# Performance work log

Measured on AMD Instinct MI355X. Metric: run time of the kernel, lower is better.

## Reference

```python
import jax, jax.numpy as jnp
import numpy as np

B, S, D = 16, 2048, 128

def setup_inputs() -> dict:
    key = jax.random.key(0)
    kq, kk, kv = jax.random.split(key, 3)
    return {
        "query": jax.random.normal(kq, (B, S, D), dtype=jnp.float32),
        "key": jax.random.normal(kk, (B, S, D), dtype=jnp.float32),
        "value": jax.random.normal(kv, (B, S, D), dtype=jnp.float32),
    }

def reference(query, key, value):
    # query: (B, S2, d), key: (B, S1, d), value: (B, S1, d)
    d_k = query.shape[-1]
    scale = 1.0 / jnp.sqrt(jnp.asarray(d_k, dtype=query.dtype))
    # (B, S2, S1) attention scores
    att = jnp.einsum('bqd,bkd->bqk', query, key) * scale
    att = jax.nn.softmax(att, axis=-1)
    # (B, S2, d_v)
    return jnp.einsum('bqk,bkd->bqd', att, value)
```

## Files before the change

kernel.cpp:

```cpp
#include <hip/hip_runtime.h>

#define B_N 16
#define S_LEN 2048
#define D_DIM 128
#define TK 32
#define NTH 32
#define PSTR 40

typedef __attribute__((ext_vector_type(16))) float f32x16;
typedef __attribute__((ext_vector_type(8)))  short short8;
typedef const __attribute__((address_space(1))) void* gp1;
typedef __attribute__((address_space(3))) void* sp3;
#define GLL(g, l) __builtin_amdgcn_global_load_lds((gp1)(const void*)(g), (sp3)(void*)(l), 16, 0, 0)

static __device__ __forceinline__ unsigned short f2bf(float f) {
  unsigned u = __builtin_bit_cast(unsigned, f);
  return (unsigned short)((u + 0x7fffu + ((u >> 16) & 1u)) >> 16);
}

__global__ __launch_bounds__(256)
void prep_kernel(const float* __restrict__ K, const float* __restrict__ V,
                 unsigned short* __restrict__ Kb, unsigned short* __restrict__ VT) {
  __shared__ unsigned short lds[64 * 66];
  int bx = blockIdx.x;
  int t  = threadIdx.x;
  if (bx < 4096) {
    size_t i = ((size_t)bx * 256 + t) * 4;
    float4 v = *(const float4*)(K + i);
    unsigned lo = (unsigned)f2bf(v.x) | ((unsigned)f2bf(v.y) << 16);
    unsigned hi = (unsigned)f2bf(v.z) | ((unsigned)f2bf(v.w) << 16);
    *(uint2*)(Kb + i) = make_uint2(lo, hi);
  } else {
    int bi = bx - 4096;
    int b  = bi & 15;
    int st = (bi >> 4) & 31;
    int dt = bi >> 9;
    const float* Vb = V + ((size_t)b * S_LEN + st * 64) * D_DIM + dt * 64;
    unsigned short* VTb = VT + ((size_t)b * D_DIM + dt * 64) * S_LEN + st * 64;
#pragma unroll
    for (int rep = 0; rep < 4; ++rep) {
      int idx = rep * 256 + t;
      int i  = idx >> 4;
      int j4 = (idx & 15) * 4;
      float4 v = *(const float4*)(Vb + (size_t)i * D_DIM + j4);
      unsigned lo = (unsigned)f2bf(v.x) | ((unsigned)f2bf(v.y) << 16);
      unsigned hi = (unsigned)f2bf(v.z) | ((unsigned)f2bf(v.w) << 16);
      *(uint2*)&lds[i * 66 + j4] = make_uint2(lo, hi);
    }
    __syncthreads();
#pragma unroll
    for (int rep = 0; rep < 4; ++rep) {
      int idx = rep * 256 + t;
      int dd = idx >> 4;
      int s4 = (idx & 15) * 4;
      unsigned short e0 = lds[(s4 + 0) * 66 + dd];
      unsigned short e1 = lds[(s4 + 1) * 66 + dd];
      unsigned short e2 = lds[(s4 + 2) * 66 + dd];
      unsigned short e3 = lds[(s4 + 3) * 66 + dd];
      *(uint2*)(VTb + (size_t)dd * S_LEN + s4) =
          make_uint2((unsigned)e0 | ((unsigned)e1 << 16),
                     (unsigned)e2 | ((unsigned)e3 << 16));
    }
  }
}

__global__ __launch_bounds__(512, 2)
void attn_kernel(const float* __restrict__ Q, const unsigned short* __restrict__ Kb,
                 const unsigned short* __restrict__ VT, float* __restrict__ O) {
  __shared__ __align__(16) char smem[86016];

  const int tid  = threadIdx.x;
  const int wave = tid >> 6;
  const int g    = wave >> 2;
  const int w4   = wave & 3;
  const int lane = tid & 63;
  const int l32  = lane & 31;
  const int half = lane >> 5;

  const int i     = blockIdx.x;
  const int b     = (i & 7) * 2 + ((i >> 3) & 1);
  const int qtile = i >> 4;
  const int qbase = qtile * 128 + w4 * 32;

  const float* Qb = Q + (size_t)b * S_LEN * D_DIM;
  const unsigned short* Kbb = Kb + (size_t)b * S_LEN * D_DIM;
  const unsigned short* VTb = VT + (size_t)b * D_DIM * S_LEN;

  unsigned short* kb0 = (unsigned short*)smem + (size_t)g * 2 * 4096;
  unsigned short* vb0 = (unsigned short*)(smem + 32768) + (size_t)g * 2 * 4096;
  unsigned short* pw  = (unsigned short*)(smem + 65536) + wave * 32 * PSTR;

  {
    const int T0 = g * NTH;
#pragma unroll
    for (int cc = 0; cc < 2; ++cc) {
      int c = w4 * 2 + cc;
      int rl = 4 * c + (lane >> 4);
      int lbk = (lane & 15) ^ (rl & 15);
      GLL(Kbb + (size_t)(T0 * TK + rl) * D_DIM + lbk * 8, kb0 + c * 512);
      int dv = 16 * c + (lane >> 2);
      int lbv = (lane & 3) ^ ((dv >> 1) & 3);
      GLL(VTb + (size_t)dv * S_LEN + T0 * TK + lbv * 8, vb0 + c * 512);
    }
  }

  short8 qa[8];
  {
    const float* qp = Qb + (size_t)(qbase + l32) * D_DIM + half * 8;
#pragma unroll
    for (int ks = 0; ks < 8; ++ks) {
      float4 a0 = *(const float4*)(qp + ks * 16);
      float4 a1 = *(const float4*)(qp + ks * 16 + 4);
      short8 f;
      f[0] = (short)f2bf(a0.x); f[1] = (short)f2bf(a0.y);
      f[2] = (short)f2bf(a0.z); f[3] = (short)f2bf(a0.w);
      f[4] = (short)f2bf(a1.x); f[5] = (short)f2bf(a1.y);
      f[6] = (short)f2bf(a1.z); f[7] = (short)f2bf(a1.w);
      qa[ks] = f;
    }
  }

  const f32x16 zf16 = {0.f,0.f,0.f,0.f,0.f,0.f,0.f,0.f,0.f,0.f,0.f,0.f,0.f,0.f,0.f,0.f};
  f32x16 oacc[4];
  float lsum[16];
#pragma unroll
  for (int dt = 0; dt < 4; ++dt) oacc[dt] = zf16;
#pragma unroll
  for (int r = 0; r < 16; ++r) lsum[r] = 0.f;

  const float SC = 0.08838834764831845f * 1.4426950408889634f;

  for (int t = 0; t < NTH; ++t) {
    __syncthreads();
    const int cb = t & 1;
    const unsigned short* kbc = kb0 + cb * 4096;
    const unsigned short* vbc = vb0 + cb * 4096;

    if (t + 1 < NTH) {
      const int nb = cb ^ 1;
      const int T = g * NTH + t + 1;
#pragma unroll
      for (int cc = 0; cc < 2; ++cc) {
        int c = w4 * 2 + cc;
        int rl = 4 * c + (lane >> 4);
        int lbk = (lane & 15) ^ (rl & 15);
        GLL(Kbb + (size_t)(T * TK + rl) * D_DIM + lbk * 8, kb0 + nb * 4096 + c * 512);
        int dv = 16 * c + (lane >> 2);
        int lbv = (lane & 3) ^ ((dv >> 1) & 3);
        GLL(VTb + (size_t)dv * S_LEN + T * TK + lbv * 8, vb0 + nb * 4096 + c * 512);
      }
    }

    f32x16 sacc = zf16;
#pragma unroll
    for (int ks = 0; ks < 8; ++ks) {
      int pk = (ks * 2 + half) ^ (l32 & 15);
      short8 kf = *(const short8*)&kbc[l32 * D_DIM + pk * 8];
      sacc = __builtin_amdgcn_mfma_f32_32x32x16_bf16(qa[ks], kf, sacc, 0, 0, 0);
    }

#pragma unroll
    for (int reg = 0; reg < 16; ++reg) {
      float p = exp2f(sacc[reg] * SC);
      lsum[reg] += p;
      int row = (reg & 3) + 8 * (reg >> 2) + 4 * half;
      pw[row * PSTR + l32] = f2bf(p);
    }

    short8 pf[2];
#pragma unroll
    for (int ks2 = 0; ks2 < 2; ++ks2)
      pf[ks2] = *(const short8*)&pw[l32 * PSTR + ks2 * 16 + half * 8];

#pragma unroll
    for (int ks2 = 0; ks2 < 2; ++ks2) {
#pragma unroll
      for (int dt = 0; dt < 4; ++dt) {
        int dv = dt * 32 + l32;
        int pv = (ks2 * 2 + half) ^ ((dv >> 1) & 3);
        short8 vf = *(const short8*)&vbc[dv * TK + pv * 8];
        oacc[dt] = __builtin_amdgcn_mfma_f32_32x32x16_bf16(pf[ks2], vf, oacc[dt], 0, 0, 0);
      }
    }
  }

#pragma unroll
  for (int reg = 0; reg < 16; ++reg) {
    float s = lsum[reg];
    s += __shfl_xor(s, 1);
    s += __shfl_xor(s, 2);
    s += __shfl_xor(s, 4);
    s += __shfl_xor(s, 8);
    s += __shfl_xor(s, 16);
    lsum[reg] = s;
  }

  __syncthreads();
  float* mo = (float*)(smem + w4 * 16512);
  float* ml = (float*)(smem + w4 * 16512 + 16384);
  if (g == 1) {
#pragma unroll
    for (int reg = 0; reg < 16; ++reg) {
      int row = (reg & 3) + 8 * (reg >> 2) + 4 * half;
#pragma unroll
      for (int dt = 0; dt < 4; ++dt)
        mo[row * 128 + dt * 32 + l32] = oacc[dt][reg];
      if (l32 == 0) ml[row] = lsum[reg];
    }
  }
  __syncthreads();
  if (g == 0) {
    float* Ob = O + (size_t)b * S_LEN * D_DIM;
#pragma unroll
    for (int reg = 0; reg < 16; ++reg) {
      int row = (reg & 3) + 8 * (reg >> 2) + 4 * half;
      float linv = 1.f / (lsum[reg] + ml[row]);
#pragma unroll
      for (int dt = 0; dt < 4; ++dt)
        Ob[(size_t)(qbase + row) * D_DIM + dt * 32 + l32] =
            (oacc[dt][reg] + mo[row * 128 + dt * 32 + l32]) * linv;
    }
  }
}

extern "C" void kernel_launch(void* const* d_in, const int* in_sizes, int n_in,
                              void* d_out, int out_size, void* d_ws, size_t ws_size,
                              hipStream_t stream) {
  const float* Q = (const float*)d_in[0];
  const float* K = (const float*)d_in[1];
  const float* V = (const float*)d_in[2];
  float* O = (float*)d_out;
  unsigned short* Kb = (unsigned short*)d_ws;
  unsigned short* VT = Kb + (size_t)B_N * S_LEN * D_DIM;
  prep_kernel<<<dim3(4096 + 1024), dim3(256), 0, stream>>>(K, V, Kb, VT);
  attn_kernel<<<dim3(256), dim3(512), 0, stream>>>(Q, Kb, VT, O);
}
```

Measured before the change: 144.3 us.

## Keep softmax probabilities in registers via transposed QK MFMA and permlane swaps

Swaps the MFMA operand order so the score tile comes out transposed, which lets each lane hold one query's scores along keys. The probabilities are packed to bf16 with v_cvt_pk_bf16_f32 and rearranged across lane halves with v_permlane32_swap to form the PV A-operand directly, removing the per-wave LDS round trip for P. The row sum also collapses to a single per-lane accumulator, and the final reduction across the 32-lane halves is one shuffle instead of 16 five-step shuffle chains. This cuts LDS traffic and shared memory size, at the cost of relying on exact MFMA register layouts and gfx950-specific inline asm.

Result: faster. 140.9 us (-2.4%).

```diff
diff --git a/kernel.cpp b/kernel.cpp
--- a/kernel.cpp
+++ b/kernel.cpp
@@ -5,10 +5,10 @@
 #define D_DIM 128
 #define TK 32
 #define NTH 32
-#define PSTR 40
 
 typedef __attribute__((ext_vector_type(16))) float f32x16;
 typedef __attribute__((ext_vector_type(8)))  short short8;
+typedef __attribute__((ext_vector_type(4)))  int   i32x4;
 typedef const __attribute__((address_space(1))) void* gp1;
 typedef __attribute__((address_space(3))) void* sp3;
 #define GLL(g, l) __builtin_amdgcn_global_load_lds((gp1)(const void*)(g), (sp3)(void*)(l), 16, 0, 0)
@@ -67,7 +67,7 @@
 __global__ __launch_bounds__(512, 2)
 void attn_kernel(const float* __restrict__ Q, const unsigned short* __restrict__ Kb,
                  const unsigned short* __restrict__ VT, float* __restrict__ O) {
-  __shared__ __align__(16) char smem[86016];
+  __shared__ __align__(16) char smem[66560];
 
   const int tid  = threadIdx.x;
   const int wave = tid >> 6;
@@ -88,7 +88,6 @@
 
   unsigned short* kb0 = (unsigned short*)smem + (size_t)g * 2 * 4096;
   unsigned short* vb0 = (unsigned short*)(smem + 32768) + (size_t)g * 2 * 4096;
-  unsigned short* pw  = (unsigned short*)(smem + 65536) + wave * 32 * PSTR;
 
   {
     const int T0 = g * NTH;
@@ -122,11 +121,9 @@
 
   const f32x16 zf16 = {0.f,0.f,0.f,0.f,0.f,0.f,0.f,0.f,0.f,0.f,0.f,0.f,0.f,0.f,0.f,0.f};
   f32x16 oacc[4];
-  float lsum[16];
+  float lsum = 0.f;
 #pragma unroll
   for (int dt = 0; dt < 4; ++dt) oacc[dt] = zf16;
-#pragma unroll
-  for (int r = 0; r < 16; ++r) lsum[r] = 0.f;
 
   const float SC = 0.08838834764831845f * 1.4426950408889634f;
 
@@ -156,21 +153,30 @@
     for (int ks = 0; ks < 8; ++ks) {
       int pk = (ks * 2 + half) ^ (l32 & 15);
       short8 kf = *(const short8*)&kbc[l32 * D_DIM + pk * 8];
-      sacc = __builtin_amdgcn_mfma_f32_32x32x16_bf16(qa[ks], kf, sacc, 0, 0, 0);
-    }
-
+      sacc = __builtin_amdgcn_mfma_f32_32x32x16_bf16(kf, qa[ks], sacc, 0, 0, 0);
+    }
+
+    float p[16];
 #pragma unroll
     for (int reg = 0; reg < 16; ++reg) {
-      float p = exp2f(sacc[reg] * SC);
-      lsum[reg] += p;
-      int row = (reg & 3) + 8 * (reg >> 2) + 4 * half;
-      pw[row * PSTR + l32] = f2bf(p);
-    }
-
+      p[reg] = exp2f(sacc[reg] * SC);
+      lsum += p[reg];
+    }
+
+    int dw[8];
+#pragma unroll
+    for (int i2 = 0; i2 < 8; ++i2)
+      asm("v_cvt_pk_bf16_f32 %0, %1, %2"
+          : "=v"(dw[i2]) : "v"(p[2 * i2]), "v"(p[2 * i2 + 1]));
+    asm("v_permlane32_swap_b32 %0, %1" : "+v"(dw[0]), "+v"(dw[2]));
+    asm("v_permlane32_swap_b32 %0, %1" : "+v"(dw[1]), "+v"(dw[3]));
+    asm("v_permlane32_swap_b32 %0, %1" : "+v"(dw[4]), "+v"(dw[6]));
+    asm("v_permlane32_swap_b32 %0, %1" : "+v"(dw[5]), "+v"(dw[7]));
+    i32x4 f0 = {dw[0], dw[1], dw[2], dw[3]};
+    i32x4 f1 = {dw[4], dw[5], dw[6], dw[7]};
     short8 pf[2];
-#pragma unroll
-    for (int ks2 = 0; ks2 < 2; ++ks2)
-      pf[ks2] = *(const short8*)&pw[l32 * PSTR + ks2 * 16 + half * 8];
+    pf[0] = __builtin_bit_cast(short8, f0);
+    pf[1] = __builtin_bit_cast(short8, f1);
 
 #pragma unroll
     for (int ks2 = 0; ks2 < 2; ++ks2) {
@@ -184,20 +190,12 @@
     }
   }
 
-#pragma unroll
-  for (int reg = 0; reg < 16; ++reg) {
-    float s = lsum[reg];
-    s += __shfl_xor(s, 1);
-    s += __shfl_xor(s, 2);
-    s += __shfl_xor(s, 4);
-    s += __shfl_xor(s, 8);
-    s += __shfl_xor(s, 16);
-    lsum[reg] = s;
-  }
+  lsum += __shfl_xor(lsum, 32);
 
   __syncthreads();
-  float* mo = (float*)(smem + w4 * 16512);
-  float* ml = (float*)(smem + w4 * 16512 + 16384);
+  float* mo  = (float*)(smem + w4 * 16640);
+  float* ml1 = (float*)(smem + w4 * 16640 + 16384);
+  float* ml0 = ml1 + 32;
   if (g == 1) {
 #pragma unroll
     for (int reg = 0; reg < 16; ++reg) {
@@ -205,8 +203,10 @@
 #pragma unroll
       for (int dt = 0; dt < 4; ++dt)
         mo[row * 128 + dt * 32 + l32] = oacc[dt][reg];
-      if (l32 == 0) ml[row] = lsum[reg];
-    }
+    }
+    if (half == 0) ml1[l32] = lsum;
+  } else {
+    if (half == 0) ml0[l32] = lsum;
   }
   __syncthreads();
   if (g == 0) {
@@ -214,7 +214,7 @@
 #pragma unroll
     for (int reg = 0; reg < 16; ++reg) {
       int row = (reg & 3) + 8 * (reg >> 2) + 4 * half;
-      float linv = 1.f / (lsum[reg] + ml[row]);
+      float linv = 1.f / (ml0[row] + ml1[row]);
 #pragma unroll
       for (int dt = 0; dt < 4; ++dt)
         Ob[(size_t)(qbase + row) * D_DIM + dt * 32 + l32] =
```
